# Kernel tuning notes

Measured on AMD Instinct MI355X. Metric: run time of the kernel, lower is better.

## Reference

```python
import jax, jax.numpy as jnp
import numpy as np

T, N, E, F_IN, H_GNN, H_OUT, RH, G, C = 8, 10000, 160000, 128, 128, 128, 128, 32, 10


def gcn_layer(x, src, dst, W, b):
    # PyG GCNConv: h = D^-1/2 (A+I) D^-1/2 (x W) + b, self-loops added, edge weight 1
    h = x @ W  # [N, H]
    ones = jnp.ones((E,), h.dtype)
    deg = jax.ops.segment_sum(ones, dst, num_segments=N) + 1.0  # +1 for self-loop
    dinv = jax.lax.rsqrt(deg)
    coef = dinv[src] * dinv[dst]  # [E]
    agg = jax.ops.segment_sum(h[src] * coef[:, None], dst, num_segments=N)
    agg = agg + h * (dinv * dinv)[:, None]  # self-loop term
    return agg + b


def snapshot_encode(x, edge_index, batch, W1, b1, W2, b2):
    src, dst = edge_index[0], edge_index[1]
    h = jax.nn.relu(gcn_layer(x, src, dst, W1, b1))
    h = jax.nn.relu(gcn_layer(h, src, dst, W2, b2))
    sums = jax.ops.segment_sum(h, batch, num_segments=G)  # global_mean_pool
    cnts = jax.ops.segment_sum(jnp.ones((N,), h.dtype), batch, num_segments=G)
    return sums / jnp.maximum(cnts, 1.0)[:, None]  # [G, H_OUT]


def gru_layer(seq, Wih, Whh, bih, bhh):
    # seq: [T, G, in]; torch nn.GRU cell equations
    H = Whh.shape[1]

    def step(h, xt):
        gi = xt @ Wih.T + bih
        gh = h @ Whh.T + bhh
        ir, iz, inn = jnp.split(gi, 3, axis=-1)
        hr, hz, hn = jnp.split(gh, 3, axis=-1)
        r = jax.nn.sigmoid(ir + hr)
        z = jax.nn.sigmoid(iz + hz)
        n = jnp.tanh(inn + r * hn)
        h_new = (1.0 - z) * n + z * h
        return h_new, h_new

    h0 = jnp.zeros((seq.shape[1], H), seq.dtype)
    hT, outs = jax.lax.scan(step, h0, seq)
    return outs, hT


def setup_inputs() -> dict:
    key = jax.random.key(0)
    ks = jax.random.split(key, 20)
    s = 0.05
    inp = {
        "x": jax.random.normal(ks[0], (T, N, F_IN), jnp.float32),
        "edge_index": jax.random.randint(ks[1], (T, 2, E), 0, N),
        "batch": jax.random.randint(ks[2], (T, N), 0, G),
        "W1": jax.random.normal(ks[3], (F_IN, H_GNN), jnp.float32) * s,
        "b1": jnp.zeros((H_GNN,), jnp.float32),
        "W2": jax.random.normal(ks[4], (H_GNN, H_OUT), jnp.float32) * s,
        "b2": jnp.zeros((H_OUT,), jnp.float32),
        "Wih0": jax.random.normal(ks[5], (3 * RH, H_OUT), jnp.float32) * s,
        "Whh0": jax.random.normal(ks[6], (3 * RH, RH), jnp.float32) * s,
        "bih0": jnp.zeros((3 * RH,), jnp.float32),
        "bhh0": jnp.zeros((3 * RH,), jnp.float32),
        "Wih1": jax.random.normal(ks[7], (3 * RH, RH), jnp.float32) * s,
        "Whh1": jax.random.normal(ks[8], (3 * RH, RH), jnp.float32) * s,
        "bih1": jnp.zeros((3 * RH,), jnp.float32),
        "bhh1": jnp.zeros((3 * RH,), jnp.float32),
        "Wc": jax.random.normal(ks[9], (C, RH), jnp.float32) * s,
        "bc": jnp.zeros((C,), jnp.float32),
    }
    return inp


def reference(x, edge_index, batch, W1, b1, W2, b2, Wih0, Whh0, bih0, bhh0,
              Wih1, Whh1, bih1, bhh1, Wc, bc):
    # per-snapshot GNN encode, vmapped over T snapshots -> [T, G, H_OUT]
    emb = jax.vmap(snapshot_encode, in_axes=(0, 0, 0, None, None, None, None))(
        x, edge_index, batch, W1, b1, W2, b2)
    outs, _ = gru_layer(emb, Wih0, Whh0, bih0, bhh0)
    _, hT = gru_layer(outs, Wih1, Whh1, bih1, bhh1)  # h_n[-1]: last layer final state
    return hT @ Wc.T + bc  # [G, C]
```

## Files before the change

### kernel.cpp

```cpp
#include <hip/hip_runtime.h>

#define T_ 8
#define N_ 10000
#define E_ 160000
#define G_ 32
#define C_ 10
#define F_ 128

typedef _Float16 f16;
typedef _Float16 f16x2 __attribute__((ext_vector_type(2)));
typedef _Float16 f16x4 __attribute__((ext_vector_type(4)));
typedef _Float16 f16x8 __attribute__((ext_vector_type(8)));
typedef float floatx4 __attribute__((ext_vector_type(4)));

static constexpr size_t ROWS = (size_t)T_ * N_;
static constexpr int SLICE = E_ / 8;

static constexpr size_t OFF_XH    = 0;
static constexpr size_t OFF_A1    = 20480000;
static constexpr size_t OFF_H1    = 40960000;
static constexpr size_t OFF_REC   = 61440000;
static constexpr size_t OFF_CNT   = 66560000;
static constexpr size_t OFF_DINV  = 69120000;
static constexpr size_t OFF_RP    = 69440000;
static constexpr size_t OFF_CNTG  = 69760032;
static constexpr size_t OFF_BRP   = 69761056;
static constexpr size_t OFF_WP    = 69762112;
static constexpr size_t OFF_BLIST = 69827648;
static constexpr size_t OFF_GPACK = 70213184;
static constexpr size_t OFF_PART  = 70999616;

__device__ __forceinline__ float sig_fast(float x) {
  return __builtin_amdgcn_rcpf(1.0f + __builtin_amdgcn_exp2f(-1.4426950408889634f * x));
}
__device__ __forceinline__ float tanh_fast(float x) {
  return 1.0f - 2.0f * __builtin_amdgcn_rcpf(1.0f + __builtin_amdgcn_exp2f(2.8853900817779268f * x));
}

__global__ __launch_bounds__(1024) void hist_kernel(const int* __restrict__ ei,
                                                    const int* __restrict__ batch,
                                                    int* __restrict__ cnt,
                                                    int* __restrict__ cntG) {
  __shared__ int hL[N_];
  __shared__ int cL[G_];
  int b = blockIdx.x, tid = threadIdx.x;
  int t = b & 7, s = b >> 3;
  for (int i = tid; i < N_; i += 1024) hL[i] = 0;
  if (tid < G_) cL[tid] = 0;
  __syncthreads();
  const int* dstp = ei + (size_t)t * 2 * E_ + E_ + s * SLICE;
  for (int e4 = tid; e4 < SLICE / 4; e4 += 1024) {
    int4 d = *(const int4*)(dstp + e4 * 4);
    atomicAdd(&hL[d.x], 1); atomicAdd(&hL[d.y], 1);
    atomicAdd(&hL[d.z], 1); atomicAdd(&hL[d.w], 1);
  }
  if (s == 0)
    for (int n = tid; n < N_; n += 1024) atomicAdd(&cL[batch[t * N_ + n]], 1);
  __syncthreads();
  int* cp = cnt + ((size_t)t * 8 + s) * N_;
  for (int i = tid; i < N_; i += 1024) cp[i] = hL[i];
  if (s == 0 && tid < G_) cntG[t * G_ + tid] = cL[tid];
}

__global__ __launch_bounds__(1024) void scan_kernel(int* __restrict__ cnt,
                                                    int* __restrict__ rp,
                                                    float* __restrict__ dinv,
                                                    const int* __restrict__ cntG,
                                                    int* __restrict__ brp) {
  __shared__ int wsum[16];
  __shared__ int carry;
  int t = blockIdx.x, tid = threadIdx.x, lane = tid & 63, wid = tid >> 6;
  if (t == 8) {
    int v = (tid < 256) ? cntG[tid] : 0;
    for (int ofs = 1; ofs < 64; ofs <<= 1) {
      int u = __shfl_up(v, ofs);
      if (lane >= ofs) v += u;
    }
    if (lane == 63 && wid < 4) wsum[wid] = v;
    __syncthreads();
    if (tid < 256) {
      int base = 0;
      for (int w = 0; w < wid; ++w) base += wsum[w];
      if (tid == 0) brp[0] = 0;
      brp[tid + 1] = v + base;
    }
    return;
  }
  if (tid == 0) { carry = 0; rp[t * (N_ + 1)] = 0; }
  __syncthreads();
  for (int c0 = 0; c0 < N_; c0 += 1024) {
    int n = c0 + tid;
    int vs[8];
    int deg = 0;
    if (n < N_) {
#pragma unroll
      for (int s = 0; s < 8; ++s) {
        vs[s] = cnt[((size_t)t * 8 + s) * N_ + n];
        deg += vs[s];
      }
      dinv[t * N_ + n] = rsqrtf((float)deg + 1.0f);
    }
    int v = (n < N_) ? deg : 0;
    int v0 = v;
    for (int ofs = 1; ofs < 64; ofs <<= 1) {
      int u = __shfl_up(v, ofs);
      if (lane >= ofs) v += u;
    }
    if (lane == 63) wsum[wid] = v;
    __syncthreads();
    if (wid == 0) {
      int w = (lane < 16) ? wsum[lane] : 0;
      for (int ofs = 1; ofs < 16; ofs <<= 1) {
        int u = __shfl_up(w, ofs);
        if (lane >= ofs) w += u;
      }
      if (lane < 16) wsum[lane] = w;
    }
    __syncthreads();
    int base = carry + (wid ? wsum[wid - 1] : 0);
    if (n < N_) {
      rp[t * (N_ + 1) + n + 1] = base + v;
      int run = base + v - v0;
#pragma unroll
      for (int s = 0; s < 8; ++s) {
        int vv = vs[s];
        cnt[((size_t)t * 8 + s) * N_ + n] = run;
        run += vv;
      }
    }
    __syncthreads();
    if (tid == 0) carry += wsum[15];
    __syncthreads();
  }
}

__global__ __launch_bounds__(1024) void fill_kernel(const int* __restrict__ ei,
                                                    const int* __restrict__ base,
                                                    int* __restrict__ rec,
                                                    const int* __restrict__ batch,
                                                    const int* __restrict__ brp,
                                                    int* __restrict__ blist) {
  __shared__ int offL[N_];
  __shared__ int cb[G_];
  int b = blockIdx.x, tid = threadIdx.x;
  int t = b & 7, s = b >> 3;
  const int* bp = base + ((size_t)t * 8 + s) * N_;
  for (int i = tid; i < N_; i += 1024) offL[i] = bp[i];
  if (s == 0 && tid < G_) cb[tid] = brp[t * G_ + tid];
  __syncthreads();
  const int* srcp = ei + (size_t)t * 2 * E_ + s * SLICE;
  const int* dstp = srcp + E_;
  int* rt = rec + (size_t)t * E_;
  for (int e4 = tid; e4 < SLICE / 4; e4 += 1024) {
    int4 sv = *(const int4*)(srcp + e4 * 4);
    int4 dv = *(const int4*)(dstp + e4 * 4);
    int p0 = atomicAdd(&offL[dv.x], 1);
    int p1 = atomicAdd(&offL[dv.y], 1);
    int p2 = atomicAdd(&offL[dv.z], 1);
    int p3 = atomicAdd(&offL[dv.w], 1);
    rt[p0] = sv.x; rt[p1] = sv.y; rt[p2] = sv.z; rt[p3] = sv.w;
  }
  if (s == 0) {
    for (int n = tid; n < N_; n += 1024) {
      int g = batch[t * N_ + n];
      int p = atomicAdd(&cb[g], 1);
      blist[p] = t * N_ + n;
    }
  }
}

__global__ void cvt_kernel(const float* __restrict__ x, const float* __restrict__ dinv,
                           f16* __restrict__ xh) {
  size_t i = ((size_t)blockIdx.x * 256 + threadIdx.x) * 4;
  float4 v = *(const float4*)(x + i);
  float d = dinv[i >> 7];
  f16x4 o; o.x = (f16)(v.x * d); o.y = (f16)(v.y * d);
  o.z = (f16)(v.z * d); o.w = (f16)(v.w * d);
  *(f16x4*)(xh + i) = o;
}

__global__ __launch_bounds__(256) void agg_kernel(const f16* __restrict__ X, f16* __restrict__ A,
                                                  const int* __restrict__ rp,
                                                  const int* __restrict__ rec,
                                                  const float* __restrict__ dinv) {
  int wave = threadIdx.x >> 6, lane = threadIdx.x & 63;
  int eg = lane >> 4;
  int cb = (lane & 15) * 8;
  int b = blockIdx.x;
  int t = b & 7, i = b >> 3;
  int n = i * 4 + wave;
  int row = t * N_ + n;
  float ds = dinv[row];
  int beg = rp[t * (N_ + 1) + n], end = rp[t * (N_ + 1) + n + 1];
  beg = __builtin_amdgcn_readfirstlane(beg);
  end = __builtin_amdgcn_readfirstlane(end);
  const int* rc = rec + (size_t)t * E_;
  const f16* Xt = X + (size_t)t * N_ * F_;

  float s[8] = {0.f, 0.f, 0.f, 0.f, 0.f, 0.f, 0.f, 0.f};
  if (eg == 3) {
    f16x8 v = *(const f16x8*)(Xt + (size_t)n * F_ + cb);
#pragma unroll
    for (int j = 0; j < 8; ++j) s[j] += (float)v[j];
  }
  int cnt = end - beg;
  int nq = cnt >> 2;
  int e = beg + eg;
  if (nq > 0) {
    int rid = rc[e];
    for (int q = 0; q + 1 < nq; ++q) {
      int nrid = rc[e + 4];
      f16x8 v = *(const f16x8*)(Xt + (size_t)rid * F_ + cb);
#pragma unroll
      for (int j = 0; j < 8; ++j) s[j] += (float)v[j];
      rid = nrid; e += 4;
    }
    f16x8 v = *(const f16x8*)(Xt + (size_t)rid * F_ + cb);
#pragma unroll
    for (int j = 0; j < 8; ++j) s[j] += (float)v[j];
    e += 4;
  }
  int rem = cnt & 3;
  if (eg < rem) {
    int rid = rc[e];
    f16x8 v = *(const f16x8*)(Xt + (size_t)rid * F_ + cb);
#pragma unroll
    for (int j = 0; j < 8; ++j) s[j] += (float)v[j];
  }
#pragma unroll
  for (int j = 0; j < 8; ++j) {
    s[j] += __shfl_xor(s[j], 16);
    s[j] += __shfl_xor(s[j], 32);
  }
  if (eg == 0) {
    f16x8 o;
#pragma unroll
    for (int j = 0; j < 8; ++j) o[j] = (f16)(ds * s[j]);
    *(f16x8*)(A + (size_t)row * F_ + cb) = o;
  }
}

__global__ void packall_kernel(const float* __restrict__ W1, const float* __restrict__ W2,
                               f16* __restrict__ Wp,
                               const float* __restrict__ A0, const float* __restrict__ A1,
                               const float* __restrict__ A2, const float* __restrict__ A3,
                               f16* __restrict__ gp) {
  int idx = blockIdx.x * 256 + threadIdx.x;
  if (idx < 32768) {
    const float* W = (idx < 16384) ? W1 : W2;
    int l = idx & 16383;
    int j = l & 7, lane = (l >> 3) & 63, ct = (l >> 9) & 7, kc = (l >> 12) & 3;
    int k = kc * 32 + ((lane >> 4) & 3) * 8 + j;
    int n = ct * 16 + (lane & 15);
    Wp[idx] = (f16)W[k * 128 + n];
  } else {
    int gidx = idx - 32768;
    int mat = gidx / 49152, l = gidx - mat * 49152;
    int j = l & 7, lane = (l >> 3) & 63, kc = (l >> 9) & 3, nt = l >> 11;
    int k = kc * 32 + ((lane >> 4) & 3) * 8 + j;
    int u = nt * 16 + (lane & 15);
    const float* W = (mat == 0) ? A0 : (mat == 1) ? A1 : (mat == 2) ? A2 : A3;
    gp[gidx] = (f16)W[u * 128 + k];
  }
}

__global__ __launch_bounds__(256) void gemm_kernel(const f16* __restrict__ A,
                                                   const f16* __restrict__ Wp,
                                                   const float* __restrict__ bias,
                                                   const float* __restrict__ scale,
                                                   f16* __restrict__ O) {
  __shared__ f16x8 Bp[2048];
  const f16x8* Wv = (const f16x8*)Wp;
  for (int i = threadIdx.x; i < 2048; i += 256) Bp[i] = Wv[i];
  __syncthreads();
  int wave = threadIdx.x >> 6, lane = threadIdx.x & 63;
  int quad = lane >> 4, m = lane & 15;
  int rowbase = blockIdx.x * 64 + wave * 16;
  const f16x8* Arow = (const f16x8*)(A + (size_t)(rowbase + m) * F_);
  floatx4 acc[8];
#pragma unroll
  for (int ct = 0; ct < 8; ++ct) { floatx4 z = {0.f, 0.f, 0.f, 0.f}; acc[ct] = z; }
#pragma unroll
  for (int kc = 0; kc < 4; ++kc) {
    f16x8 a = Arow[kc * 4 + quad];
#pragma unroll
    for (int ct = 0; ct < 8; ++ct)
      acc[ct] = __builtin_amdgcn_mfma_f32_16x16x32_f16(a, Bp[(kc * 8 + ct) * 64 + lane],
                                                       acc[ct], 0, 0, 0);
  }
  float sv[4];
#pragma unroll
  for (int r = 0; r < 4; ++r)
    sv[r] = scale ? scale[rowbase + quad * 4 + r] : 1.0f;
#pragma unroll
  for (int ct = 0; ct < 8; ++ct) {
    int colc = ct * 16 + m;
    float bv = bias[colc];
#pragma unroll
    for (int r = 0; r < 4; ++r) {
      int row = rowbase + quad * 4 + r;
      float v = fmaxf(acc[ct][r] + bv, 0.0f) * sv[r];
      O[(size_t)row * F_ + colc] = (f16)v;
    }
  }
}

__global__ void pool1_kernel(const f16* __restrict__ H, const int* __restrict__ brp,
                             const int* __restrict__ blist, float* __restrict__ part) {
  int b = blockIdx.x;
  int wave = threadIdx.x >> 6, lane = threadIdx.x & 63;
  int idx = b >> 1;
  int s = (b & 1) * 4 + wave;
  int beg = brp[idx], end = brp[idx + 1];
  beg = __builtin_amdgcn_readfirstlane(beg);
  end = __builtin_amdgcn_readfirstlane(end);
  int len = end - beg;
  int lo = beg + (int)(((long long)len * s) >> 3);
  int hi = beg + (int)(((long long)len * (s + 1)) >> 3);
  float a00 = 0.f, a01 = 0.f, a10 = 0.f, a11 = 0.f;
  float a20 = 0.f, a21 = 0.f, a30 = 0.f, a31 = 0.f;
  int e = lo;
  for (; e + 3 < hi; e += 4) {
    int r0 = blist[e], r1 = blist[e + 1], r2 = blist[e + 2], r3 = blist[e + 3];
    f16x2 v0 = *(const f16x2*)(H + (size_t)r0 * F_ + 2 * lane);
    f16x2 v1 = *(const f16x2*)(H + (size_t)r1 * F_ + 2 * lane);
    f16x2 v2 = *(const f16x2*)(H + (size_t)r2 * F_ + 2 * lane);
    f16x2 v3 = *(const f16x2*)(H + (size_t)r3 * F_ + 2 * lane);
    a00 += (float)v0.x; a01 += (float)v0.y;
    a10 += (float)v1.x; a11 += (float)v1.y;
    a20 += (float)v2.x; a21 += (float)v2.y;
    a30 += (float)v3.x; a31 += (float)v3.y;
  }
  for (; e < hi; ++e) {
    int r = blist[e];
    f16x2 v = *(const f16x2*)(H + (size_t)r * F_ + 2 * lane);
    a00 += (float)v.x; a01 += (float)v.y;
  }
  float2 o;
  o.x = (a00 + a10) + (a20 + a30);
  o.y = (a01 + a11) + (a21 + a31);
  *(float2*)(part + ((size_t)idx * 8 + s) * F_ + 2 * lane) = o;
}

__global__ __launch_bounds__(256, 1) void gru_mega(
    const f16* __restrict__ gp, const float* __restrict__ part,
    const int* __restrict__ brp,
    const float* __restrict__ bih0, const float* __restrict__ bhh0,
    const float* __restrict__ bih1, const float* __restrict__ bhh1,
    const float* __restrict__ Wc, const float* __restrict__ bc,
    float* __restrict__ out) {
  __shared__ f16 emb_l[16][136];
  __shared__ float gib0[16][384];
  __shared__ f16 hb0[16 * 136];
  __shared__ f16 hb1[16 * 136];
  __shared__ float ghb[2 * 384];
  __shared__ float gib[2 * 384];
  __shared__ float h1s[2 * 128];
  int tid = threadIdx.x, wave = tid >> 6, lane = tid & 63;
  int quad = lane >> 4, mm = lane & 15;
  int g2 = tid >> 7, f = tid & 127;
  int bid = blockIdx.x;

  {
    int r = tid >> 4;
    int fb = (tid & 15) * 8;
    int idx = (r >> 1) * G_ + bid * 2 + (r & 1);
    float s[8] = {0.f, 0.f, 0.f, 0.f, 0.f, 0.f, 0.f, 0.f};
#pragma unroll
    for (int k = 0; k < 8; ++k) {
      const float* p = part + ((size_t)idx * 8 + k) * F_ + fb;
      float4 v0 = *(const float4*)p;
      float4 v1 = *(const float4*)(p + 4);
      s[0] += v0.x; s[1] += v0.y; s[2] += v0.z; s[3] += v0.w;
      s[4] += v1.x; s[5] += v1.y; s[6] += v1.z; s[7] += v1.w;
    }
    float d = fmaxf((float)(brp[idx + 1] - brp[idx]), 1.0f);
    f16x8 ev;
#pragma unroll
    for (int j = 0; j < 8; ++j) ev[j] = (f16)(s[j] / d);
    *(f16x8*)(&emb_l[r][fb]) = ev;
  }
  __syncthreads();

  {
    floatx4 acc[6];
#pragma unroll
    for (int i = 0; i < 6; ++i) { floatx4 z = {0.f, 0.f, 0.f, 0.f}; acc[i] = z; }
#pragma unroll
    for (int kc = 0; kc < 4; ++kc) {
      f16x8 a = *(const f16x8*)(&emb_l[mm][kc * 32 + quad * 8]);
#pragma unroll
      for (int i = 0; i < 6; ++i) {
        int nt = wave * 6 + i;
        f16x8 bf = *(const f16x8*)(gp + (size_t)((nt * 4 + kc) * 64 + lane) * 8);
        acc[i] = __builtin_amdgcn_mfma_f32_16x16x32_f16(a, bf, acc[i], 0, 0, 0);
      }
    }
#pragma unroll
    for (int i = 0; i < 6; ++i)
#pragma unroll
      for (int r = 0; r < 4; ++r)
        gib0[quad * 4 + r][(wave * 6 + i) * 16 + mm] = acc[i][r];
  }

  f16x8 B0[24], B1[24];
#pragma unroll
  for (int i = 0; i < 6; ++i)
#pragma unroll
    for (int kc = 0; kc < 4; ++kc) {
      size_t off = (size_t)((((wave * 6 + i) * 4 + kc) * 64 + lane)) * 8;
      B0[i * 4 + kc] = *(const f16x8*)(gp + 1 * 49152 + off);
      B1[i * 4 + kc] = *(const f16x8*)(gp + 3 * 49152 + off);
    }
  float br0 = bih0[f] + bhh0[f];
  float bz0 = bih0[128 + f] + bhh0[128 + f];
  float bni0 = bih0[256 + f], bnh0 = bhh0[256 + f];
  float br1 = bih1[f] + bhh1[f];
  float bz1 = bih1[128 + f] + bhh1[128 + f];
  float bni1 = bih1[256 + f], bnh1 = bhh1[256 + f];

  for (int i = tid; i < 16 * 136; i += 256) { hb0[i] = (f16)0.f; hb1[i] = (f16)0.f; }
  float h0 = 0.f, h1 = 0.f;
  __syncthreads();

  const f16* wih1 = gp + 2 * 49152;
  for (int t = 0; t < T_; ++t) {
    f16x8 Bs[24];
#pragma unroll
    for (int i = 0; i < 6; ++i)
#pragma unroll
      for (int kc = 0; kc < 4; ++kc)
        Bs[i * 4 + kc] = *(const f16x8*)(wih1 +
            (size_t)((((wave * 6 + i) * 4 + kc) * 64 + lane)) * 8);
    const float* gi = &gib0[t * 2 + g2][0];
    float gir = gi[f], giz = gi[128 + f], gin = gi[256 + f];

    floatx4 acc[6];
#pragma unroll
    for (int i = 0; i < 6; ++i) { floatx4 z = {0.f, 0.f, 0.f, 0.f}; acc[i] = z; }
#pragma unroll
    for (int kc = 0; kc < 4; ++kc) {
      f16x8 a = *(const f16x8*)(hb0 + mm * 136 + kc * 32 + quad * 8);
#pragma unroll
      for (int i = 0; i < 6; ++i)
        acc[i] = __builtin_amdgcn_mfma_f32_16x16x32_f16(a, B0[i * 4 + kc], acc[i], 0, 0, 0);
    }
    if (quad == 0) {
#pragma unroll
      for (int i = 0; i < 6; ++i) {
        ghb[0 * 384 + wave * 96 + i * 16 + mm] = acc[i][0];
        ghb[1 * 384 + wave * 96 + i * 16 + mm] = acc[i][1];
      }
    }
    __syncthreads();

    {
      float hr = ghb[g2 * 384 + f];
      float hz = ghb[g2 * 384 + 128 + f];
      float hn = ghb[g2 * 384 + 256 + f];
      float r = sig_fast(gir + hr + br0);
      float z = sig_fast(giz + hz + bz0);
      float nn = tanh_fast(gin + bni0 + r * (hn + bnh0));
      h0 = (1.0f - z) * nn + z * h0;
      hb0[g2 * 136 + f] = (f16)h0;
    }
    __syncthreads();

    floatx4 accx[6], acch[6];
#pragma unroll
    for (int i = 0; i < 6; ++i) {
      floatx4 z = {0.f, 0.f, 0.f, 0.f}; accx[i] = z; acch[i] = z;
    }
#pragma unroll
    for (int kc = 0; kc < 4; ++kc) {
      f16x8 ax = *(const f16x8*)(hb0 + mm * 136 + kc * 32 + quad * 8);
      f16x8 ah = *(const f16x8*)(hb1 + mm * 136 + kc * 32 + quad * 8);
#pragma unroll
      for (int i = 0; i < 6; ++i) {
        accx[i] = __builtin_amdgcn_mfma_f32_16x16x32_f16(ax, Bs[i * 4 + kc], accx[i], 0, 0, 0);
        acch[i] = __builtin_amdgcn_mfma_f32_16x16x32_f16(ah, B1[i * 4 + kc], acch[i], 0, 0, 0);
      }
    }
    if (quad == 0) {
#pragma unroll
      for (int i = 0; i < 6; ++i) {
        gib[0 * 384 + wave * 96 + i * 16 + mm] = accx[i][0];
        gib[1 * 384 + wave * 96 + i * 16 + mm] = accx[i][1];
        ghb[0 * 384 + wave * 96 + i * 16 + mm] = acch[i][0];
        ghb[1 * 384 + wave * 96 + i * 16 + mm] = acch[i][1];
      }
    }
    __syncthreads();

    {
      float i1r = gib[g2 * 384 + f];
      float i1z = gib[g2 * 384 + 128 + f];
      float i1n = gib[g2 * 384 + 256 + f];
      float hr = ghb[g2 * 384 + f];
      float hz = ghb[g2 * 384 + 128 + f];
      float hn = ghb[g2 * 384 + 256 + f];
      float r = sig_fast(i1r + hr + br1);
      float z = sig_fast(i1z + hz + bz1);
      float nn = tanh_fast(i1n + bni1 + r * (hn + bnh1));
      h1 = (1.0f - z) * nn + z * h1;
      hb1[g2 * 136 + f] = (f16)h1;
    }
    __syncthreads();
  }

  h1s[g2 * 128 + f] = h1;
  __syncthreads();
  if (tid < 2 * C_) {
    int gg = tid / C_, c = tid - gg * C_;
    float s = bc[c];
    const float* wr = Wc + (size_t)c * 128;
    const float* hr = h1s + gg * 128;
    for (int k = 0; k < 128; k += 4) {
      float4 w = *(const float4*)(wr + k);
      s += hr[k] * w.x + hr[k + 1] * w.y + hr[k + 2] * w.z + hr[k + 3] * w.w;
    }
    out[(bid * 2 + gg) * C_ + c] = s;
  }
}

extern "C" void kernel_launch(void* const* d_in, const int* in_sizes, int n_in,
                              void* d_out, int out_size, void* d_ws, size_t ws_size,
                              hipStream_t stream) {
  const float* x    = (const float*)d_in[0];
  const int*   ei   = (const int*)d_in[1];
  const int*   batch= (const int*)d_in[2];
  const float* W1   = (const float*)d_in[3];
  const float* b1   = (const float*)d_in[4];
  const float* W2   = (const float*)d_in[5];
  const float* b2   = (const float*)d_in[6];
  const float* Wih0 = (const float*)d_in[7];
  const float* Whh0 = (const float*)d_in[8];
  const float* bih0 = (const float*)d_in[9];
  const float* bhh0 = (const float*)d_in[10];
  const float* Wih1 = (const float*)d_in[11];
  const float* Whh1 = (const float*)d_in[12];
  const float* bih1 = (const float*)d_in[13];
  const float* bhh1 = (const float*)d_in[14];
  const float* Wc   = (const float*)d_in[15];
  const float* bc   = (const float*)d_in[16];
  float* out = (float*)d_out;

  char* ws = (char*)d_ws;
  f16*   Xh    = (f16*)(ws + OFF_XH);
  f16*   A1    = (f16*)(ws + OFF_A1);
  f16*   H1    = (f16*)(ws + OFF_H1);
  f16*   A2    = A1;
  f16*   H2    = Xh;
  int*   rec   = (int*)(ws + OFF_REC);
  int*   cnt   = (int*)(ws + OFF_CNT);
  float* dinv  = (float*)(ws + OFF_DINV);
  int*   rp    = (int*)(ws + OFF_RP);
  int*   cntG  = (int*)(ws + OFF_CNTG);
  int*   brp   = (int*)(ws + OFF_BRP);
  f16*   Wp    = (f16*)(ws + OFF_WP);
  int*   blist = (int*)(ws + OFF_BLIST);
  f16*   gp    = (f16*)(ws + OFF_GPACK);
  float* part  = (float*)(ws + OFF_PART);

  packall_kernel<<<896, 256, 0, stream>>>(W1, W2, Wp, Wih0, Whh0, Wih1, Whh1, gp);
  hist_kernel<<<64, 1024, 0, stream>>>(ei, batch, cnt, cntG);
  scan_kernel<<<9, 1024, 0, stream>>>(cnt, rp, dinv, cntG, brp);
  cvt_kernel<<<10000, 256, 0, stream>>>(x, dinv, Xh);
  fill_kernel<<<64, 1024, 0, stream>>>(ei, cnt, rec, batch, brp, blist);

  agg_kernel<<<20000, 256, 0, stream>>>(Xh, A1, rp, rec, dinv);
  gemm_kernel<<<1250, 256, 0, stream>>>(A1, Wp, b1, dinv, H1);
  agg_kernel<<<20000, 256, 0, stream>>>(H1, A2, rp, rec, dinv);
  gemm_kernel<<<1250, 256, 0, stream>>>(A2, Wp + 16384, b2, (const float*)nullptr, H2);

  pool1_kernel<<<512, 256, 0, stream>>>(H2, brp, blist, part);
  gru_mega<<<16, 256, 0, stream>>>(gp, part, brp, bih0, bhh0, bih1, bhh1, Wc, bc, out);
}
```

Before: 297.8 us.

## Fuse mean-pool into second GEMM via atomics and retune CSR/aggregation split

Removes the batch-list construction and the separate pool kernel. The second GEMM epilogue now atomically accumulates ReLU outputs into 32 per-graph partial slots, which are zeroed in the pack kernel, and the GRU kernel reads the counts directly. Edge histogram and fill now use 16 slices per snapshot instead of 8. The aggregation kernel splits each node's 128 features across two waves with 8 edge groups per wave and prefetches one step ahead. Float atomics add contention and make the pooled sums nondeterministic, and twice as many aggregation blocks are launched.

```diff
diff --git a/kernel.cpp b/kernel.cpp
--- a/kernel.cpp
+++ b/kernel.cpp
@@ -13,22 +13,21 @@
 typedef _Float16 f16x8 __attribute__((ext_vector_type(8)));
 typedef float floatx4 __attribute__((ext_vector_type(4)));
 
-static constexpr size_t ROWS = (size_t)T_ * N_;
-static constexpr int SLICE = E_ / 8;
+static constexpr int NSLICE = 16;
+static constexpr int SLICE = E_ / NSLICE;
+static constexpr int PSL = 32;
 
 static constexpr size_t OFF_XH    = 0;
 static constexpr size_t OFF_A1    = 20480000;
 static constexpr size_t OFF_H1    = 40960000;
 static constexpr size_t OFF_REC   = 61440000;
 static constexpr size_t OFF_CNT   = 66560000;
-static constexpr size_t OFF_DINV  = 69120000;
-static constexpr size_t OFF_RP    = 69440000;
-static constexpr size_t OFF_CNTG  = 69760032;
-static constexpr size_t OFF_BRP   = 69761056;
-static constexpr size_t OFF_WP    = 69762112;
-static constexpr size_t OFF_BLIST = 69827648;
-static constexpr size_t OFF_GPACK = 70213184;
-static constexpr size_t OFF_PART  = 70999616;
+static constexpr size_t OFF_DINV  = 71680000;
+static constexpr size_t OFF_RP    = 72000000;
+static constexpr size_t OFF_CNTG  = 72320128;
+static constexpr size_t OFF_WP    = 72321280;
+static constexpr size_t OFF_GPACK = 72386816;
+static constexpr size_t OFF_PART  = 72780032;
 
 __device__ __forceinline__ float sig_fast(float x) {
   return __builtin_amdgcn_rcpf(1.0f + __builtin_amdgcn_exp2f(-1.4426950408889634f * x));
@@ -57,45 +56,27 @@
   if (s == 0)
     for (int n = tid; n < N_; n += 1024) atomicAdd(&cL[batch[t * N_ + n]], 1);
   __syncthreads();
-  int* cp = cnt + ((size_t)t * 8 + s) * N_;
+  int* cp = cnt + ((size_t)t * NSLICE + s) * N_;
   for (int i = tid; i < N_; i += 1024) cp[i] = hL[i];
   if (s == 0 && tid < G_) cntG[t * G_ + tid] = cL[tid];
 }
 
 __global__ __launch_bounds__(1024) void scan_kernel(int* __restrict__ cnt,
                                                     int* __restrict__ rp,
-                                                    float* __restrict__ dinv,
-                                                    const int* __restrict__ cntG,
-                                                    int* __restrict__ brp) {
+                                                    float* __restrict__ dinv) {
   __shared__ int wsum[16];
   __shared__ int carry;
   int t = blockIdx.x, tid = threadIdx.x, lane = tid & 63, wid = tid >> 6;
-  if (t == 8) {
-    int v = (tid < 256) ? cntG[tid] : 0;
-    for (int ofs = 1; ofs < 64; ofs <<= 1) {
-      int u = __shfl_up(v, ofs);
-      if (lane >= ofs) v += u;
-    }
-    if (lane == 63 && wid < 4) wsum[wid] = v;
-    __syncthreads();
-    if (tid < 256) {
-      int base = 0;
-      for (int w = 0; w < wid; ++w) base += wsum[w];
-      if (tid == 0) brp[0] = 0;
-      brp[tid + 1] = v + base;
-    }
-    return;
-  }
   if (tid == 0) { carry = 0; rp[t * (N_ + 1)] = 0; }
   __syncthreads();
   for (int c0 = 0; c0 < N_; c0 += 1024) {
     int n = c0 + tid;
-    int vs[8];
+    int vs[NSLICE];
     int deg = 0;
     if (n < N_) {
 #pragma unroll
-      for (int s = 0; s < 8; ++s) {
-        vs[s] = cnt[((size_t)t * 8 + s) * N_ + n];
+      for (int s = 0; s < NSLICE; ++s) {
+        vs[s] = cnt[((size_t)t * NSLICE + s) * N_ + n];
         deg += vs[s];
       }
       dinv[t * N_ + n] = rsqrtf((float)deg + 1.0f);
@@ -122,9 +103,9 @@
       rp[t * (N_ + 1) + n + 1] = base + v;
       int run = base + v - v0;
 #pragma unroll
-      for (int s = 0; s < 8; ++s) {
+      for (int s = 0; s < NSLICE; ++s) {
         int vv = vs[s];
-        cnt[((size_t)t * 8 + s) * N_ + n] = run;
+        cnt[((size_t)t * NSLICE + s) * N_ + n] = run;
         run += vv;
       }
     }
@@ -136,17 +117,12 @@
 
 __global__ __launch_bounds__(1024) void fill_kernel(const int* __restrict__ ei,
                                                     const int* __restrict__ base,
-                                                    int* __restrict__ rec,
-                                                    const int* __restrict__ batch,
-                                                    const int* __restrict__ brp,
-                                                    int* __restrict__ blist) {
+                                                    int* __restrict__ rec) {
   __shared__ int offL[N_];
-  __shared__ int cb[G_];
   int b = blockIdx.x, tid = threadIdx.x;
   int t = b & 7, s = b >> 3;
-  const int* bp = base + ((size_t)t * 8 + s) * N_;
+  const int* bp = base + ((size_t)t * NSLICE + s) * N_;
   for (int i = tid; i < N_; i += 1024) offL[i] = bp[i];
-  if (s == 0 && tid < G_) cb[tid] = brp[t * G_ + tid];
   __syncthreads();
   const int* srcp = ei + (size_t)t * 2 * E_ + s * SLICE;
   const int* dstp = srcp + E_;
@@ -160,13 +136,6 @@
     int p3 = atomicAdd(&offL[dv.w], 1);
     rt[p0] = sv.x; rt[p1] = sv.y; rt[p2] = sv.z; rt[p3] = sv.w;
   }
-  if (s == 0) {
-    for (int n = tid; n < N_; n += 1024) {
-      int g = batch[t * N_ + n];
-      int p = atomicAdd(&cb[g], 1);
-      blist[p] = t * N_ + n;
-    }
-  }
 }
 
 __global__ void cvt_kernel(const float* __restrict__ x, const float* __restrict__ dinv,
@@ -184,51 +153,54 @@
                                                   const int* __restrict__ rec,
                                                   const float* __restrict__ dinv) {
   int wave = threadIdx.x >> 6, lane = threadIdx.x & 63;
-  int eg = lane >> 4;
-  int cb = (lane & 15) * 8;
+  int eg = lane >> 3;
+  int hf = wave & 1;
+  int cb = hf * 64 + (lane & 7) * 8;
   int b = blockIdx.x;
-  int t = b & 7, i = b >> 3;
-  int n = i * 4 + wave;
+  int t = b & 7, pair = b >> 3;
+  int n = pair * 2 + (wave >> 1);
   int row = t * N_ + n;
   float ds = dinv[row];
   int beg = rp[t * (N_ + 1) + n], end = rp[t * (N_ + 1) + n + 1];
   beg = __builtin_amdgcn_readfirstlane(beg);
   end = __builtin_amdgcn_readfirstlane(end);
-  const int* rc = rec + (size_t)t * E_;
+  const int* rcb = rec + (size_t)t * E_ + beg + eg;
   const f16* Xt = X + (size_t)t * N_ * F_;
 
   float s[8] = {0.f, 0.f, 0.f, 0.f, 0.f, 0.f, 0.f, 0.f};
-  if (eg == 3) {
+  if (eg == 7) {
     f16x8 v = *(const f16x8*)(Xt + (size_t)n * F_ + cb);
 #pragma unroll
     for (int j = 0; j < 8; ++j) s[j] += (float)v[j];
   }
   int cnt = end - beg;
-  int nq = cnt >> 2;
-  int e = beg + eg;
+  int nq = cnt >> 3;
   if (nq > 0) {
-    int rid = rc[e];
-    for (int q = 0; q + 1 < nq; ++q) {
-      int nrid = rc[e + 4];
-      f16x8 v = *(const f16x8*)(Xt + (size_t)rid * F_ + cb);
+    int rid = rcb[0];
+    f16x8 v = *(const f16x8*)(Xt + (size_t)rid * F_ + cb);
+    int ridn = 0;
+    if (nq > 1) ridn = rcb[8];
+    for (int q = 1; q < nq; ++q) {
+      f16x8 vn = *(const f16x8*)(Xt + (size_t)ridn * F_ + cb);
+      int ridnn = 0;
+      if (q + 1 < nq) ridnn = rcb[(q + 1) * 8];
 #pragma unroll
       for (int j = 0; j < 8; ++j) s[j] += (float)v[j];
-      rid = nrid; e += 4;
-    }
+      v = vn; ridn = ridnn;
+    }
+#pragma unroll
+    for (int j = 0; j < 8; ++j) s[j] += (float)v[j];
+  }
+  int rem = cnt & 7;
+  if (eg < rem) {
+    int rid = rcb[nq * 8];
     f16x8 v = *(const f16x8*)(Xt + (size_t)rid * F_ + cb);
 #pragma unroll
     for (int j = 0; j < 8; ++j) s[j] += (float)v[j];
-    e += 4;
-  }
-  int rem = cnt & 3;
-  if (eg < rem) {
-    int rid = rc[e];
-    f16x8 v = *(const f16x8*)(Xt + (size_t)rid * F_ + cb);
-#pragma unroll
-    for (int j = 0; j < 8; ++j) s[j] += (float)v[j];
   }
 #pragma unroll
   for (int j = 0; j < 8; ++j) {
+    s[j] += __shfl_xor(s[j], 8);
     s[j] += __shfl_xor(s[j], 16);
     s[j] += __shfl_xor(s[j], 32);
   }
@@ -244,8 +216,10 @@
                                f16* __restrict__ Wp,
                                const float* __restrict__ A0, const float* __restrict__ A1,
                                const float* __restrict__ A2, const float* __restrict__ A3,
-                               f16* __restrict__ gp) {
+                               f16* __restrict__ gp, float4* __restrict__ part4) {
   int idx = blockIdx.x * 256 + threadIdx.x;
+  float4 z = {0.f, 0.f, 0.f, 0.f};
+  part4[idx] = z;
   if (idx < 32768) {
     const float* W = (idx < 16384) ? W1 : W2;
     int l = idx & 16383;
@@ -253,7 +227,7 @@
     int k = kc * 32 + ((lane >> 4) & 3) * 8 + j;
     int n = ct * 16 + (lane & 15);
     Wp[idx] = (f16)W[k * 128 + n];
-  } else {
+  } else if (idx < 229376) {
     int gidx = idx - 32768;
     int mat = gidx / 49152, l = gidx - mat * 49152;
     int j = l & 7, lane = (l >> 3) & 63, kc = (l >> 9) & 3, nt = l >> 11;
@@ -264,11 +238,14 @@
   }
 }
 
+template <int POOL>
 __global__ __launch_bounds__(256) void gemm_kernel(const f16* __restrict__ A,
                                                    const f16* __restrict__ Wp,
                                                    const float* __restrict__ bias,
                                                    const float* __restrict__ scale,
-                                                   f16* __restrict__ O) {
+                                                   f16* __restrict__ O,
+                                                   const int* __restrict__ batch,
+                                                   float* __restrict__ part) {
   __shared__ f16x8 Bp[2048];
   const f16x8* Wv = (const f16x8*)Wp;
   for (int i = threadIdx.x; i < 2048; i += 256) Bp[i] = Wv[i];
@@ -288,63 +265,47 @@
       acc[ct] = __builtin_amdgcn_mfma_f32_16x16x32_f16(a, Bp[(kc * 8 + ct) * 64 + lane],
                                                        acc[ct], 0, 0, 0);
   }
-  float sv[4];
-#pragma unroll
-  for (int r = 0; r < 4; ++r)
-    sv[r] = scale ? scale[rowbase + quad * 4 + r] : 1.0f;
-#pragma unroll
-  for (int ct = 0; ct < 8; ++ct) {
-    int colc = ct * 16 + m;
-    float bv = bias[colc];
+  if (POOL == 0) {
+    float sv[4];
+#pragma unroll
+    for (int r = 0; r < 4; ++r) sv[r] = scale[rowbase + quad * 4 + r];
+#pragma unroll
+    for (int ct = 0; ct < 8; ++ct) {
+      int colc = ct * 16 + m;
+      float bv = bias[colc];
+#pragma unroll
+      for (int r = 0; r < 4; ++r) {
+        int row = rowbase + quad * 4 + r;
+        float v = fmaxf(acc[ct][r] + bv, 0.0f) * sv[r];
+        O[(size_t)row * F_ + colc] = (f16)v;
+      }
+    }
+  } else {
+    int sl = (blockIdx.x * 4 + wave) & (PSL - 1);
+    size_t pb[4];
 #pragma unroll
     for (int r = 0; r < 4; ++r) {
       int row = rowbase + quad * 4 + r;
-      float v = fmaxf(acc[ct][r] + bv, 0.0f) * sv[r];
-      O[(size_t)row * F_ + colc] = (f16)v;
-    }
-  }
-}
-
-__global__ void pool1_kernel(const f16* __restrict__ H, const int* __restrict__ brp,
-                             const int* __restrict__ blist, float* __restrict__ part) {
-  int b = blockIdx.x;
-  int wave = threadIdx.x >> 6, lane = threadIdx.x & 63;
-  int idx = b >> 1;
-  int s = (b & 1) * 4 + wave;
-  int beg = brp[idx], end = brp[idx + 1];
-  beg = __builtin_amdgcn_readfirstlane(beg);
-  end = __builtin_amdgcn_readfirstlane(end);
-  int len = end - beg;
-  int lo = beg + (int)(((long long)len * s) >> 3);
-  int hi = beg + (int)(((long long)len * (s + 1)) >> 3);
-  float a00 = 0.f, a01 = 0.f, a10 = 0.f, a11 = 0.f;
-  float a20 = 0.f, a21 = 0.f, a30 = 0.f, a31 = 0.f;
-  int e = lo;
-  for (; e + 3 < hi; e += 4) {
-    int r0 = blist[e], r1 = blist[e + 1], r2 = blist[e + 2], r3 = blist[e + 3];
-    f16x2 v0 = *(const f16x2*)(H + (size_t)r0 * F_ + 2 * lane);
-    f16x2 v1 = *(const f16x2*)(H + (size_t)r1 * F_ + 2 * lane);
-    f16x2 v2 = *(const f16x2*)(H + (size_t)r2 * F_ + 2 * lane);
-    f16x2 v3 = *(const f16x2*)(H + (size_t)r3 * F_ + 2 * lane);
-    a00 += (float)v0.x; a01 += (float)v0.y;
-    a10 += (float)v1.x; a11 += (float)v1.y;
-    a20 += (float)v2.x; a21 += (float)v2.y;
-    a30 += (float)v3.x; a31 += (float)v3.y;
-  }
-  for (; e < hi; ++e) {
-    int r = blist[e];
-    f16x2 v = *(const f16x2*)(H + (size_t)r * F_ + 2 * lane);
-    a00 += (float)v.x; a01 += (float)v.y;
-  }
-  float2 o;
-  o.x = (a00 + a10) + (a20 + a30);
-  o.y = (a01 + a11) + (a21 + a31);
-  *(float2*)(part + ((size_t)idx * 8 + s) * F_ + 2 * lane) = o;
+      int t = row / N_;
+      int g = batch[row];
+      pb[r] = ((size_t)(t * G_ + g) * PSL + sl) * F_;
+    }
+#pragma unroll
+    for (int ct = 0; ct < 8; ++ct) {
+      int colc = ct * 16 + m;
+      float bv = bias[colc];
+#pragma unroll
+      for (int r = 0; r < 4; ++r) {
+        float v = fmaxf(acc[ct][r] + bv, 0.0f);
+        atomicAdd(&part[pb[r] + colc], v);
+      }
+    }
+  }
 }
 
 __global__ __launch_bounds__(256, 1) void gru_mega(
     const f16* __restrict__ gp, const float* __restrict__ part,
-    const int* __restrict__ brp,
+    const int* __restrict__ cntG,
     const float* __restrict__ bih0, const float* __restrict__ bhh0,
     const float* __restrict__ bih1, const float* __restrict__ bhh1,
     const float* __restrict__ Wc, const float* __restrict__ bc,
@@ -366,15 +327,15 @@
     int fb = (tid & 15) * 8;
     int idx = (r >> 1) * G_ + bid * 2 + (r & 1);
     float s[8] = {0.f, 0.f, 0.f, 0.f, 0.f, 0.f, 0.f, 0.f};
-#pragma unroll
-    for (int k = 0; k < 8; ++k) {
-      const float* p = part + ((size_t)idx * 8 + k) * F_ + fb;
+#pragma unroll 4
+    for (int k = 0; k < PSL; ++k) {
+      const float* p = part + ((size_t)idx * PSL + k) * F_ + fb;
       float4 v0 = *(const float4*)p;
       float4 v1 = *(const float4*)(p + 4);
       s[0] += v0.x; s[1] += v0.y; s[2] += v0.z; s[3] += v0.w;
       s[4] += v1.x; s[5] += v1.y; s[6] += v1.z; s[7] += v1.w;
     }
-    float d = fmaxf((float)(brp[idx + 1] - brp[idx]), 1.0f);
+    float d = fmaxf((float)cntG[idx], 1.0f);
     f16x8 ev;
 #pragma unroll
     for (int j = 0; j < 8; ++j) ev[j] = (f16)(s[j] / d);
@@ -550,29 +511,26 @@
   f16*   A1    = (f16*)(ws + OFF_A1);
   f16*   H1    = (f16*)(ws + OFF_H1);
   f16*   A2    = A1;
-  f16*   H2    = Xh;
   int*   rec   = (int*)(ws + OFF_REC);
   int*   cnt   = (int*)(ws + OFF_CNT);
   float* dinv  = (float*)(ws + OFF_DINV);
   int*   rp    = (int*)(ws + OFF_RP);
   int*   cntG  = (int*)(ws + OFF_CNTG);
-  int*   brp   = (int*)(ws + OFF_BRP);
   f16*   Wp    = (f16*)(ws + OFF_WP);
-  int*   blist = (int*)(ws + OFF_BLIST);
   f16*   gp    = (f16*)(ws + OFF_GPACK);
   float* part  = (float*)(ws + OFF_PART);
 
-  packall_kernel<<<896, 256, 0, stream>>>(W1, W2, Wp, Wih0, Whh0, Wih1, Whh1, gp);
-  hist_kernel<<<64, 1024, 0, stream>>>(ei, batch, cnt, cntG);
-  scan_kernel<<<9, 1024, 0, stream>>>(cnt, rp, dinv, cntG, brp);
+  packall_kernel<<<1024, 256, 0, stream>>>(W1, W2, Wp, Wih0, Whh0, Wih1, Whh1, gp,
+                                           (float4*)part);
+  hist_kernel<<<8 * NSLICE, 1024, 0, stream>>>(ei, batch, cnt, cntG);
+  scan_kernel<<<8, 1024, 0, stream>>>(cnt, rp, dinv);
   cvt_kernel<<<10000, 256, 0, stream>>>(x, dinv, Xh);
-  fill_kernel<<<64, 1024, 0, stream>>>(ei, cnt, rec, batch, brp, blist);
-
-  agg_kernel<<<20000, 256, 0, stream>>>(Xh, A1, rp, rec, dinv);
-  gemm_kernel<<<1250, 256, 0, stream>>>(A1, Wp, b1, dinv, H1);
-  agg_kernel<<<20000, 256, 0, stream>>>(H1, A2, rp, rec, dinv);
-  gemm_kernel<<<1250, 256, 0, stream>>>(A2, Wp + 16384, b2, (const float*)nullptr, H2);
-
-  pool1_kernel<<<512, 256, 0, stream>>>(H2, brp, blist, part);
-  gru_mega<<<16, 256, 0, stream>>>(gp, part, brp, bih0, bhh0, bih1, bhh1, Wc, bc, out);
-}
+  fill_kernel<<<8 * NSLICE, 1024, 0, stream>>>(ei, cnt, rec);
+
+  agg_kernel<<<40000, 256, 0, stream>>>(Xh, A1, rp, rec, dinv);
+  gemm_kernel<0><<<1250, 256, 0, stream>>>(A1, Wp, b1, dinv, H1, nullptr, nullptr);
+  agg_kernel<<<40000, 256, 0, stream>>>(H1, A2, rp, rec, dinv);
+  gemm_kernel<1><<<1250, 256, 0, stream>>>(A2, Wp + 16384, b2, nullptr, nullptr, batch, part);
+
+  gru_mega<<<16, 256, 0, stream>>>(gp, part, cntG, bih0, bhh0, bih1, bhh1, Wc, bc, out);
+}
```

Measured after the change: 349.0 us. 17.2% more time.

## Merge prep kernels via block-range dispatch and deepen gather prefetch in aggregation

Applied to the files above, without the earlier changes.

The weight-packing kernel now shares a launch with the degree histogram: extra blocks appended to the grid do the packing. Likewise, the fp16 feature conversion shares a launch with the CSR fill kernel. This removes two kernel launches and lets independent work overlap within a single grid. The aggregation loop now keeps two feature loads and one index load in flight instead of one of each, to better hide gather latency, at the cost of more registers per thread. The 1024-thread conversion blocks also reserve the large shared array declared for the fill path, which may limit how many of them fit on a CU at once.

```diff
diff --git a/kernel.cpp b/kernel.cpp
--- a/kernel.cpp
+++ b/kernel.cpp
@@ -37,13 +37,41 @@
   return 1.0f - 2.0f * __builtin_amdgcn_rcpf(1.0f + __builtin_amdgcn_exp2f(2.8853900817779268f * x));
 }
 
-__global__ __launch_bounds__(1024) void hist_kernel(const int* __restrict__ ei,
-                                                    const int* __restrict__ batch,
-                                                    int* __restrict__ cnt,
-                                                    int* __restrict__ cntG) {
+__global__ __launch_bounds__(1024) void prep0_kernel(const int* __restrict__ ei,
+                                                     const int* __restrict__ batch,
+                                                     int* __restrict__ cnt,
+                                                     int* __restrict__ cntG,
+                                                     const float* __restrict__ W1,
+                                                     const float* __restrict__ W2,
+                                                     f16* __restrict__ Wp,
+                                                     const float* __restrict__ A0,
+                                                     const float* __restrict__ A1,
+                                                     const float* __restrict__ A2,
+                                                     const float* __restrict__ A3,
+                                                     f16* __restrict__ gp) {
   __shared__ int hL[N_];
   __shared__ int cL[G_];
   int b = blockIdx.x, tid = threadIdx.x;
+  if (b >= 64) {
+    int idx = (b - 64) * 1024 + tid;
+    if (idx < 32768) {
+      const float* W = (idx < 16384) ? W1 : W2;
+      int l = idx & 16383;
+      int j = l & 7, lane = (l >> 3) & 63, ct = (l >> 9) & 7, kc = (l >> 12) & 3;
+      int k = kc * 32 + ((lane >> 4) & 3) * 8 + j;
+      int n = ct * 16 + (lane & 15);
+      Wp[idx] = (f16)W[k * 128 + n];
+    } else {
+      int gidx = idx - 32768;
+      int mat = gidx / 49152, l = gidx - mat * 49152;
+      int j = l & 7, lane = (l >> 3) & 63, kc = (l >> 9) & 3, nt = l >> 11;
+      int k = kc * 32 + ((lane >> 4) & 3) * 8 + j;
+      int u = nt * 16 + (lane & 15);
+      const float* W = (mat == 0) ? A0 : (mat == 1) ? A1 : (mat == 2) ? A2 : A3;
+      gp[gidx] = (f16)W[u * 128 + k];
+    }
+    return;
+  }
   int t = b & 7, s = b >> 3;
   for (int i = tid; i < N_; i += 1024) hL[i] = 0;
   if (tid < G_) cL[tid] = 0;
@@ -134,15 +162,27 @@
   }
 }
 
-__global__ __launch_bounds__(1024) void fill_kernel(const int* __restrict__ ei,
-                                                    const int* __restrict__ base,
-                                                    int* __restrict__ rec,
-                                                    const int* __restrict__ batch,
-                                                    const int* __restrict__ brp,
-                                                    int* __restrict__ blist) {
+__global__ __launch_bounds__(1024) void cvtfill_kernel(const int* __restrict__ ei,
+                                                       const int* __restrict__ base,
+                                                       int* __restrict__ rec,
+                                                       const int* __restrict__ batch,
+                                                       const int* __restrict__ brp,
+                                                       int* __restrict__ blist,
+                                                       const float* __restrict__ x,
+                                                       const float* __restrict__ dinv,
+                                                       f16* __restrict__ xh) {
   __shared__ int offL[N_];
   __shared__ int cb[G_];
   int b = blockIdx.x, tid = threadIdx.x;
+  if (b >= 64) {
+    size_t i = ((size_t)(b - 64) * 1024 + tid) * 4;
+    float4 v = *(const float4*)(x + i);
+    float d = dinv[i >> 7];
+    f16x4 o; o.x = (f16)(v.x * d); o.y = (f16)(v.y * d);
+    o.z = (f16)(v.z * d); o.w = (f16)(v.w * d);
+    *(f16x4*)(xh + i) = o;
+    return;
+  }
   int t = b & 7, s = b >> 3;
   const int* bp = base + ((size_t)t * 8 + s) * N_;
   for (int i = tid; i < N_; i += 1024) offL[i] = bp[i];
@@ -167,16 +207,6 @@
       blist[p] = t * N_ + n;
     }
   }
-}
-
-__global__ void cvt_kernel(const float* __restrict__ x, const float* __restrict__ dinv,
-                           f16* __restrict__ xh) {
-  size_t i = ((size_t)blockIdx.x * 256 + threadIdx.x) * 4;
-  float4 v = *(const float4*)(x + i);
-  float d = dinv[i >> 7];
-  f16x4 o; o.x = (f16)(v.x * d); o.y = (f16)(v.y * d);
-  o.z = (f16)(v.z * d); o.w = (f16)(v.w * d);
-  *(f16x4*)(xh + i) = o;
 }
 
 __global__ __launch_bounds__(256) void agg_kernel(const f16* __restrict__ X, f16* __restrict__ A,
@@ -194,7 +224,7 @@
   int beg = rp[t * (N_ + 1) + n], end = rp[t * (N_ + 1) + n + 1];
   beg = __builtin_amdgcn_readfirstlane(beg);
   end = __builtin_amdgcn_readfirstlane(end);
-  const int* rc = rec + (size_t)t * E_;
+  const int* rcb = rec + (size_t)t * E_ + beg + eg;
   const f16* Xt = X + (size_t)t * N_ * F_;
 
   float s[8] = {0.f, 0.f, 0.f, 0.f, 0.f, 0.f, 0.f, 0.f};
@@ -205,24 +235,30 @@
   }
   int cnt = end - beg;
   int nq = cnt >> 2;
-  int e = beg + eg;
   if (nq > 0) {
-    int rid = rc[e];
-    for (int q = 0; q + 1 < nq; ++q) {
-      int nrid = rc[e + 4];
-      f16x8 v = *(const f16x8*)(Xt + (size_t)rid * F_ + cb);
-#pragma unroll
-      for (int j = 0; j < 8; ++j) s[j] += (float)v[j];
-      rid = nrid; e += 4;
-    }
-    f16x8 v = *(const f16x8*)(Xt + (size_t)rid * F_ + cb);
-#pragma unroll
-    for (int j = 0; j < 8; ++j) s[j] += (float)v[j];
-    e += 4;
+    int ridA = rcb[0];
+    int ridB = (nq > 1) ? rcb[4] : 0;
+    int ridC = (nq > 2) ? rcb[8] : 0;
+    f16x8 vA = *(const f16x8*)(Xt + (size_t)ridA * F_ + cb);
+    f16x8 vB;
+    if (nq > 1) vB = *(const f16x8*)(Xt + (size_t)ridB * F_ + cb);
+    for (int q = 0; q + 2 < nq; ++q) {
+      f16x8 vC = *(const f16x8*)(Xt + (size_t)ridC * F_ + cb);
+      int ridD = rcb[(q + 3) * 4];
+#pragma unroll
+      for (int j = 0; j < 8; ++j) s[j] += (float)vA[j];
+      vA = vB; vB = vC; ridC = ridD;
+    }
+#pragma unroll
+    for (int j = 0; j < 8; ++j) s[j] += (float)vA[j];
+    if (nq > 1) {
+#pragma unroll
+      for (int j = 0; j < 8; ++j) s[j] += (float)vB[j];
+    }
   }
   int rem = cnt & 3;
   if (eg < rem) {
-    int rid = rc[e];
+    int rid = rcb[nq * 4];
     f16x8 v = *(const f16x8*)(Xt + (size_t)rid * F_ + cb);
 #pragma unroll
     for (int j = 0; j < 8; ++j) s[j] += (float)v[j];
@@ -237,30 +273,6 @@
 #pragma unroll
     for (int j = 0; j < 8; ++j) o[j] = (f16)(ds * s[j]);
     *(f16x8*)(A + (size_t)row * F_ + cb) = o;
-  }
-}
-
-__global__ void packall_kernel(const float* __restrict__ W1, const float* __restrict__ W2,
-                               f16* __restrict__ Wp,
-                               const float* __restrict__ A0, const float* __restrict__ A1,
-                               const float* __restrict__ A2, const float* __restrict__ A3,
-                               f16* __restrict__ gp) {
-  int idx = blockIdx.x * 256 + threadIdx.x;
-  if (idx < 32768) {
-    const float* W = (idx < 16384) ? W1 : W2;
-    int l = idx & 16383;
-    int j = l & 7, lane = (l >> 3) & 63, ct = (l >> 9) & 7, kc = (l >> 12) & 3;
-    int k = kc * 32 + ((lane >> 4) & 3) * 8 + j;
-    int n = ct * 16 + (lane & 15);
-    Wp[idx] = (f16)W[k * 128 + n];
-  } else {
-    int gidx = idx - 32768;
-    int mat = gidx / 49152, l = gidx - mat * 49152;
-    int j = l & 7, lane = (l >> 3) & 63, kc = (l >> 9) & 3, nt = l >> 11;
-    int k = kc * 32 + ((lane >> 4) & 3) * 8 + j;
-    int u = nt * 16 + (lane & 15);
-    const float* W = (mat == 0) ? A0 : (mat == 1) ? A1 : (mat == 2) ? A2 : A3;
-    gp[gidx] = (f16)W[u * 128 + k];
   }
 }
 
@@ -562,11 +574,10 @@
   f16*   gp    = (f16*)(ws + OFF_GPACK);
   float* part  = (float*)(ws + OFF_PART);
 
-  packall_kernel<<<896, 256, 0, stream>>>(W1, W2, Wp, Wih0, Whh0, Wih1, Whh1, gp);
-  hist_kernel<<<64, 1024, 0, stream>>>(ei, batch, cnt, cntG);
+  prep0_kernel<<<288, 1024, 0, stream>>>(ei, batch, cnt, cntG,
+                                         W1, W2, Wp, Wih0, Whh0, Wih1, Whh1, gp);
   scan_kernel<<<9, 1024, 0, stream>>>(cnt, rp, dinv, cntG, brp);
-  cvt_kernel<<<10000, 256, 0, stream>>>(x, dinv, Xh);
-  fill_kernel<<<64, 1024, 0, stream>>>(ei, cnt, rec, batch, brp, blist);
+  cvtfill_kernel<<<2564, 1024, 0, stream>>>(ei, cnt, rec, batch, brp, blist, x, dinv, Xh);
 
   agg_kernel<<<20000, 256, 0, stream>>>(Xh, A1, rp, rec, dinv);
   gemm_kernel<<<1250, 256, 0, stream>>>(A1, Wp, b1, dinv, H1);
```

Result: no change. 293.4 us (-1.5%).
